# Kernel optimization log

Hardware: AMD Instinct MI355X
Metric: run time of the kernel (lower is better)

## Reference

```python
import jax, jax.numpy as jnp
from jax import lax
import numpy as np

INPUT_DIM = 1024; ENT_DIM = 256; KEY_DIM = 32; FUNC_DIM = 256; HID = 32
NUM_LAYERS = 1; UNIT_TYPE_DIM = 259; MAX_ENT = 64; B = 256; N = 512
NEG = 1e9

def _ln(x, g, b, eps=1e-5):
    m = x.mean(-1, keepdims=True)
    v = ((x - m) ** 2).mean(-1, keepdims=True)
    return (x - m) / jnp.sqrt(v + eps) * g + b

def setup_inputs() -> dict:
    key = jax.random.key(0)
    ks = jax.random.split(key, 16)
    def lin(k, i, o, s=0.02):
        return jax.random.normal(k, (i, o), jnp.float32) * s, jnp.zeros((o,), jnp.float32)
    p = {}
    p['key_fc_w'], p['key_fc_b'] = lin(ks[0], ENT_DIM, KEY_DIM)
    p['func_fc_w'], p['func_fc_b'] = lin(ks[1], UNIT_TYPE_DIM, FUNC_DIM)
    p['fc1_w'], p['fc1_b'] = lin(ks[2], INPUT_DIM, FUNC_DIM)
    p['fc2_w'], p['fc2_b'] = lin(ks[3], FUNC_DIM, KEY_DIM)
    p['embed_fc_w'], p['embed_fc_b'] = lin(ks[4], KEY_DIM, INPUT_DIM)
    p['lstm_wx'] = jax.random.normal(ks[5], (NUM_LAYERS, KEY_DIM, 4 * HID), jnp.float32) * 0.05
    p['lstm_wh'] = jax.random.normal(ks[6], (NUM_LAYERS, HID, 4 * HID), jnp.float32) * 0.05
    p['lstm_b'] = jnp.zeros((NUM_LAYERS, 4 * HID), jnp.float32)
    p['lstm_ln_gx'] = jnp.ones((NUM_LAYERS, 4 * HID), jnp.float32)
    p['lstm_ln_bx'] = jnp.zeros((NUM_LAYERS, 4 * HID), jnp.float32)
    p['lstm_ln_gh'] = jnp.ones((NUM_LAYERS, 4 * HID), jnp.float32)
    p['lstm_ln_bh'] = jnp.zeros((NUM_LAYERS, 4 * HID), jnp.float32)
    inp = {
        'embedding': jax.random.normal(ks[7], (B, INPUT_DIM), jnp.float32),
        'available_unit_type_mask': (jax.random.uniform(ks[8], (B, UNIT_TYPE_DIM)) < 0.5).astype(jnp.float32),
        'available_units_mask': jnp.ones((B, N), jnp.float32),
        'entity_embedding': jax.random.normal(ks[9], (B, N, ENT_DIM), jnp.float32),
        'temperature': jnp.float32(1.0),
    }
    inp.update(p)
    return inp

def reference(embedding, available_unit_type_mask, available_units_mask, entity_embedding,
              temperature, key_fc_w, key_fc_b, func_fc_w, func_fc_b, fc1_w, fc1_b,
              fc2_w, fc2_b, embed_fc_w, embed_fc_b, lstm_wx, lstm_wh, lstm_b,
              lstm_ln_gx, lstm_ln_bx, lstm_ln_gh, lstm_ln_bh):
    relu = jax.nn.relu
    # _get_key: [B,N,KEY] + end-flag row of zeros -> [B,N+1,KEY]
    key = entity_embedding @ key_fc_w + key_fc_b
    key = jnp.concatenate([key, jnp.zeros((B, 1, KEY_DIM), key.dtype)], axis=1)
    end_idx = N
    # _get_init_query
    func_embed = relu(available_unit_type_mask @ func_fc_w + func_fc_b)
    x0 = relu(embedding @ fc1_w + fc1_b)
    x0 = relu((x0 + func_embed) @ fc2_w + fc2_b)  # [B, KEY_DIM]
    mask0 = jnp.concatenate([available_units_mask, jnp.ones((B, 1), available_units_mask.dtype)], axis=1)

    h0 = jnp.zeros((NUM_LAYERS, B, HID), key.dtype)
    c0 = jnp.zeros((NUM_LAYERS, B, HID), key.dtype)
    units0 = jnp.zeros((B, N + 1), jnp.int32)
    done0 = jnp.zeros((B,), bool)
    rng0 = jax.random.key(42)

    def step(carry, _):
        x, h, c, mask, units, done, rng = carry
        xi = x
        hs, cs = [], []
        for l in range(NUM_LAYERS):  # LN-LSTM, gate order i,f,o,u (DI-engine)
            gate = (_ln(xi @ lstm_wx[l], lstm_ln_gx[l], lstm_ln_bx[l])
                    + _ln(h[l] @ lstm_wh[l], lstm_ln_gh[l], lstm_ln_bh[l]) + lstm_b[l])
            i_g, f_g, o_g, u_g = jnp.split(gate, 4, axis=-1)
            cl = jax.nn.sigmoid(f_g) * c[l] + jax.nn.sigmoid(i_g) * jnp.tanh(u_g)
            hl = jax.nn.sigmoid(o_g) * jnp.tanh(cl)
            hs.append(hl); cs.append(cl); xi = hl
        h_new = jnp.stack(hs); c_new = jnp.stack(cs)
        q = (xi[:, None, :] * key).mean(-1)          # [B, N+1] pointer scores
        q = q - (1.0 - mask) * NEG
        rng, sk = jax.random.split(rng)
        idx = jax.random.categorical(sk, q / temperature, axis=-1)  # [B]
        is_end = idx == end_idx
        active = jnp.logical_not(done)
        sel = active & jnp.logical_not(is_end)
        onehot = jax.nn.one_hot(idx, N + 1, dtype=mask.dtype)
        units = jnp.where(sel[:, None] & (onehot > 0.5), 1, units)
        mask = jnp.where(sel[:, None], mask * (1.0 - onehot), mask)
        done = done | (active & is_end)
        return (xi, h_new, c_new, mask, units, done, rng), (q, active)

    carry, (logits, valid) = lax.scan(step, (x0, h0, c0, mask0, units0, done0, rng0), None, length=MAX_ENT)
    units = carry[4]
    emb_sel = (units[..., None].astype(key.dtype) * key).mean(axis=1)  # [B, KEY_DIM]
    emb_sel = emb_sel @ embed_fc_w + embed_fc_b
    return logits, valid, units, embedding + emb_sel
```

## Files before the change

kernel.cpp:

```cpp
#include <hip/hip_runtime.h>
#include <stdint.h>
#include <stddef.h>

#define JAX_PARTITIONABLE 1

#define B_   256
#define N_   512
#define NP_  513
#define KROW 516
#define T_   64
#define CS   4
#define NCH  16
#define NEGC 1e9f

__host__ __device__ __forceinline__ void tf2x32(uint32_t k0, uint32_t k1,
    uint32_t x0, uint32_t x1, uint32_t& o0, uint32_t& o1) {
  const uint32_t k2 = k0 ^ k1 ^ 0x1BD11BDAu;
#define TFR(r) { x0 += x1; x1 = (x1 << (r)) | (x1 >> (32 - (r))); x1 ^= x0; }
  x0 += k0; x1 += k1;
  TFR(13) TFR(15) TFR(26) TFR(6)
  x0 += k1; x1 += k2 + 1u;
  TFR(17) TFR(29) TFR(16) TFR(24)
  x0 += k2; x1 += k0 + 2u;
  TFR(13) TFR(15) TFR(26) TFR(6)
  x0 += k0; x1 += k1 + 3u;
  TFR(17) TFR(29) TFR(16) TFR(24)
  x0 += k1; x1 += k2 + 4u;
  TFR(13) TFR(15) TFR(26) TFR(6)
  x0 += k2; x1 += k0 + 5u;
#undef TFR
  o0 = x0; o1 = x1;
}

struct SkKeys { uint32_t k[128]; };

static SkKeys compute_chain() {
  SkKeys s;
  uint32_t r0 = 0u, r1 = 42u;
  for (int t = 0; t < 64; ++t) {
#if JAX_PARTITIONABLE
    uint32_t a0, a1, b0, b1;
    tf2x32(r0, r1, 0u, 0u, a0, a1);
    tf2x32(r0, r1, 0u, 1u, b0, b1);
    s.k[2*t] = b0; s.k[2*t+1] = b1;
    r0 = a0; r1 = a1;
#else
    uint32_t p0, p1, q0, q1;
    tf2x32(r0, r1, 0u, 2u, p0, p1);
    tf2x32(r0, r1, 1u, 3u, q0, q1);
    s.k[2*t] = p1; s.k[2*t+1] = q1;
    r0 = p0; r1 = q0;
#endif
  }
  return s;
}

__device__ __forceinline__ float gumbel_draw(uint32_t k0, uint32_t k1, int b, int n) {
  uint32_t bits;
#if JAX_PARTITIONABLE
  uint32_t j = (uint32_t)(b * NP_ + n);
  uint32_t o0, o1; tf2x32(k0, k1, 0u, j, o0, o1);
  bits = o0 ^ o1;
#else
  int j = b * NP_ + n;
  uint32_t o0, o1;
  if (j < 65664) { tf2x32(k0, k1, (uint32_t)j, (uint32_t)(j + 65664), o0, o1); bits = o0; }
  else           { tf2x32(k0, k1, (uint32_t)(j - 65664), (uint32_t)j, o0, o1); bits = o1; }
#endif
  float f = __uint_as_float((bits >> 9) | 0x3F800000u) - 1.0f;
  const float TINY = 1.17549435e-38f;
  float u = fmaxf(TINY, f + TINY);
  return -logf(-logf(u));
}

__device__ __forceinline__ float sigm(float x) {
  return 0.5f + 0.5f * tanhf(0.5f * x);
}

__device__ __forceinline__ void bar_lds() {
  asm volatile("s_waitcnt lgkmcnt(0)\n\ts_barrier" ::: "memory");
}

#define OFF_KEY   0
#define OFF_H     16512
#define OFF_Q     18560
#define OFF_G     22688
#define OFF_UNITS 33008
#define OFF_SK    33524
#define OFF_ES    33652
#define OFF_PART  33684
#define OFF_T     34196
#define OFF_X0    34452
#define LDS_FLOATS 34484

__global__ void __launch_bounds__(512, 2)
suh_fused(const float* __restrict__ emb, const float* __restrict__ autm,
          const float* __restrict__ aum, const float* __restrict__ ent,
          const float* __restrict__ temp_p,
          const float* __restrict__ key_w, const float* __restrict__ key_b,
          const float* __restrict__ func_w, const float* __restrict__ func_b,
          const float* __restrict__ fc1_w, const float* __restrict__ fc1_b,
          const float* __restrict__ fc2_w, const float* __restrict__ fc2_b,
          const float* __restrict__ emb_w, const float* __restrict__ emb_b,
          const float* __restrict__ wx, const float* __restrict__ wh,
          const float* __restrict__ lstm_bb,
          const float* __restrict__ ln_gx, const float* __restrict__ ln_bx,
          const float* __restrict__ ln_gh, const float* __restrict__ ln_bh,
          float* __restrict__ out_logits, float* __restrict__ out_valid,
          float* __restrict__ out_units, float* __restrict__ out_final,
          SkKeys sk)
{
  extern __shared__ __align__(16) float sm[];
  int* smi = (int*)sm;
  const int b   = blockIdx.x;
  const int tid = threadIdx.x;
  const int L   = tid - 64;

  const float temp = temp_p[0];

  if (tid < 256) {
    float a = 0.f;
    const float* e = emb + (size_t)b * 1024;
    #pragma unroll 8
    for (int k = 0; k < 1024; ++k) a += e[k] * fc1_w[k * 256 + tid];
    a = fmaxf(a + fc1_b[tid], 0.f);
    float f = 0.f;
    const float* m = autm + (size_t)b * 259;
    for (int k = 0; k < 259; ++k) f += m[k] * func_w[k * 256 + tid];
    f = fmaxf(f + func_b[tid], 0.f);
    sm[OFF_T + tid] = a + f;
  } else {
    if (tid < 384) smi[OFF_SK + (tid - 256)] = (int)sk.k[tid - 256];
    if (tid >= 480) sm[OFF_KEY + (tid - 480) * KROW + N_] = 0.f;
  }
  __syncthreads();

  if (tid < 32) {
    float s = 0.f;
    #pragma unroll 8
    for (int m2 = 0; m2 < 256; ++m2) s += sm[OFF_T + m2] * fc2_w[m2 * 32 + tid];
    sm[OFF_X0 + tid] = fmaxf(s + fc2_b[tid], 0.f);
  }
  __syncthreads();

  float kr0[32], kr1[32];
  float mreg[8], ureg[8];
  float m512 = 1.0f;
  int done_reg = 0;

  auto qprep = [&](int cc, int qs) {
    const int qb = OFF_Q + qs * (CS * 516);
    #pragma unroll 1
    for (int tl = 0; tl < CS; ++tl) {
      const int hb = OFF_H + (cc * CS + tl) * 32;
      float hv[32];
      #pragma unroll
      for (int r = 0; r < 8; ++r) {
        float4 v = *(const float4*)&sm[hb + r * 4];
        hv[r*4] = v.x; hv[r*4+1] = v.y; hv[r*4+2] = v.z; hv[r*4+3] = v.w;
      }
      float a0 = 0.f;
      #pragma unroll
      for (int k = 0; k < 32; ++k) a0 += hv[k] * kr0[k];
      sm[qb + tl * 516 + L] = a0 * (1.0f / 32.0f);
      if (L < 64) {
        float a1 = 0.f;
        #pragma unroll
        for (int k = 0; k < 32; ++k) a1 += hv[k] * kr1[k];
        sm[qb + tl * 516 + L + 448] = a1 * (1.0f / 32.0f);
      }
    }
  };
  auto gprep = [&](int cc, int gs) {
    const int gb = OFF_G + gs * (CS * 516);
    #pragma unroll 1
    for (int i = 0; i < 5; ++i) {
      const int idx = i * 448 + L;
      if (idx < CS * 512) {
        const int tl = idx >> 9, n = idx & 511;
        const int t = cc * CS + tl;
        sm[gb + tl * 516 + n] =
            gumbel_draw((uint32_t)smi[OFF_SK + 2*t], (uint32_t)smi[OFF_SK + 2*t + 1], b, n);
      }
    }
    if (L < CS) {
      const int t = cc * CS + L;
      sm[gb + L * 516 + N_] =
          gumbel_draw((uint32_t)smi[OFF_SK + 2*t], (uint32_t)smi[OFF_SK + 2*t + 1], b, N_);
    }
  };

  if (tid < 64) {
    float wxr0[32], wxr1[32], whr0[32], whr1[32];
    #pragma unroll
    for (int k = 0; k < 32; ++k) {
      wxr0[k] = wx[k * 128 + tid];
      wxr1[k] = wx[k * 128 + 64 + tid];
      whr0[k] = wh[k * 128 + tid];
      whr1[k] = wh[k * 128 + 64 + tid];
    }
    #pragma unroll
    for (int k = 0; k < 32; ++k) {
      asm volatile("" : "+v"(wxr0[k]), "+v"(wxr1[k]), "+v"(whr0[k]), "+v"(whr1[k]));
    }
    const float gxg0 = ln_gx[tid], gxg1 = ln_gx[tid + 64];
    const float gxb0 = ln_bx[tid], gxb1 = ln_bx[tid + 64];
    const float ghg0 = ln_gh[tid], ghg1 = ln_gh[tid + 64];
    const float ghb0 = ln_bh[tid], ghb1 = ln_bh[tid + 64];
    const float lb0  = lstm_bb[tid], lb1 = lstm_bb[tid + 64];

    float xf[32];
    #pragma unroll
    for (int r = 0; r < 8; ++r) {
      float4 v = *(const float4*)&sm[OFF_X0 + r * 4];
      xf[r*4] = v.x; xf[r*4+1] = v.y; xf[r*4+2] = v.z; xf[r*4+3] = v.w;
    }
    float creg = 0.f;

    #pragma unroll 1
    for (int t = 0; t < T_; ++t) {
      float a0 = 0.f, a1 = 0.f, b0 = 0.f, b1 = 0.f;
      #pragma unroll
      for (int k = 0; k < 32; ++k) { a0 += xf[k] * wxr0[k]; a1 += xf[k] * wxr1[k]; }
      if (t > 0) {
        #pragma unroll
        for (int k = 0; k < 32; ++k) { b0 += xf[k] * whr0[k]; b1 += xf[k] * whr1[k]; }
      }
      float sx = a0 + a1, sh = b0 + b1;
      for (int off = 32; off; off >>= 1) {
        sx += __shfl_down(sx, off);
        sh += __shfl_down(sh, off);
      }
      float mx  = __shfl(sx, 0) * (1.0f / 128.0f);
      float mh2 = __shfl(sh, 0) * (1.0f / 128.0f);
      float dx0 = a0 - mx, dx1 = a1 - mx;
      float dh0 = b0 - mh2, dh1 = b1 - mh2;
      float ssx = dx0 * dx0 + dx1 * dx1;
      float ssh = dh0 * dh0 + dh1 * dh1;
      for (int off = 32; off; off >>= 1) {
        ssx += __shfl_down(ssx, off);
        ssh += __shfl_down(ssh, off);
      }
      float vx = __shfl(ssx, 0) * (1.0f / 128.0f);
      float vh = __shfl(ssh, 0) * (1.0f / 128.0f);
      float rx = 1.0f / sqrtf(vx + 1e-5f);
      float rh = 1.0f / sqrtf(vh + 1e-5f);
      float lnx0 = dx0 * rx * gxg0 + gxb0;
      float lnx1 = dx1 * rx * gxg1 + gxb1;
      float lnh0 = dh0 * rh * ghg0 + ghb0;
      float lnh1 = dh1 * rh * ghg1 + ghb1;
      float g0 = lnx0 + lnh0 + lb0;
      float g1 = lnx1 + lnh1 + lb1;
      float fq = __shfl(g0, tid + 32);
      float uq = __shfl(g1, tid + 32);
      float cN = sigm(fq) * creg + sigm(g0) * tanhf(uq);
      float hN = sigm(g1) * tanhf(cN);
      creg = cN;
      if (tid < 32) sm[OFF_H + t * 32 + tid] = hN;
      #pragma unroll
      for (int k = 0; k < 32; ++k) xf[k] = __shfl(hN, k);
    }
  } else {
    const float4* kw4 = (const float4*)key_w;
    {
      const float4* er = (const float4*)(ent + ((size_t)b * N_ + L) * 256);
      float acc[32];
      #pragma unroll
      for (int c = 0; c < 32; ++c) acc[c] = 0.f;
      #pragma unroll 1
      for (int k4 = 0; k4 < 64; ++k4) {
        float4 ev = er[k4];
        float e4[4] = {ev.x, ev.y, ev.z, ev.w};
        #pragma unroll
        for (int j = 0; j < 4; ++j) {
          const int k = k4 * 4 + j;
          #pragma unroll
          for (int c4 = 0; c4 < 8; ++c4) {
            float4 w = kw4[k * 8 + c4];
            acc[c4*4+0] += e4[j] * w.x;
            acc[c4*4+1] += e4[j] * w.y;
            acc[c4*4+2] += e4[j] * w.z;
            acc[c4*4+3] += e4[j] * w.w;
          }
        }
      }
      #pragma unroll
      for (int c = 0; c < 32; ++c) {
        kr0[c] = acc[c] + key_b[c];
        sm[OFF_KEY + c * KROW + L] = kr0[c];
      }
    }
    if (L < 64) {
      const int n = L + 448;
      const float4* er = (const float4*)(ent + ((size_t)b * N_ + n) * 256);
      float acc[32];
      #pragma unroll
      for (int c = 0; c < 32; ++c) acc[c] = 0.f;
      #pragma unroll 1
      for (int k4 = 0; k4 < 64; ++k4) {
        float4 ev = er[k4];
        float e4[4] = {ev.x, ev.y, ev.z, ev.w};
        #pragma unroll
        for (int j = 0; j < 4; ++j) {
          const int k = k4 * 4 + j;
          #pragma unroll
          for (int c4 = 0; c4 < 8; ++c4) {
            float4 w = kw4[k * 8 + c4];
            acc[c4*4+0] += e4[j] * w.x;
            acc[c4*4+1] += e4[j] * w.y;
            acc[c4*4+2] += e4[j] * w.z;
            acc[c4*4+3] += e4[j] * w.w;
          }
        }
      }
      #pragma unroll
      for (int c = 0; c < 32; ++c) {
        kr1[c] = acc[c] + key_b[c];
        sm[OFF_KEY + c * KROW + n] = kr1[c];
      }
    }
    #pragma unroll
    for (int k = 0; k < 32; ++k) {
      asm volatile("" : "+v"(kr0[k]), "+v"(kr1[k]));
    }
    #pragma unroll 1
    for (int cc = 0; cc < 4; ++cc) gprep(cc, cc);
  }
  __syncthreads();

  if (tid < 64) {
    #pragma unroll
    for (int j = 0; j < 8; ++j) {
      mreg[j] = aum[(size_t)b * N_ + tid + 64 * j];
      ureg[j] = 0.f;
    }
  } else {
    qprep(0, 0);
  }
  bar_lds();

  for (int c = 0; c < NCH; ++c) {
    if (tid < 64) {
      const int qbase = OFF_Q + (c & 1) * (CS * 516);
      const int gbase = OFF_G + (c % 5) * (CS * 516);
      #pragma unroll 1
      for (int tl = 0; tl < CS; ++tl) {
        const int t = c * CS + tl;
        float* lrow = out_logits + ((size_t)t * B_ + b) * NP_;
        float bv = 0.f; int bi = 0;
        #pragma unroll
        for (int j = 0; j < 8; ++j) {
          const int n = tid + 64 * j;
          float q = sm[qbase + tl * 516 + n] - (1.0f - mreg[j]) * NEGC;
          lrow[n] = q;
          float v = q / temp + sm[gbase + tl * 516 + n];
          if (j == 0) { bv = v; bi = n; }
          else if (v > bv) { bv = v; bi = n; }
        }
        if (tid == 0) {
          float q = -(1.0f - m512) * NEGC;
          lrow[N_] = q;
          float v = q / temp + sm[gbase + tl * 516 + N_];
          if (v > bv) { bv = v; bi = N_; }
        }
        for (int off = 32; off; off >>= 1) {
          float ov = __shfl_down(bv, off);
          int   oi = __shfl_down(bi, off);
          if (ov > bv || (ov == bv && oi < bi)) { bv = ov; bi = oi; }
        }
        const int sel_i = __shfl(bi, 0);
        const int active = !done_reg;
        const int is_end = (sel_i == N_);
        if (tid == 0) out_valid[(size_t)t * B_ + b] = active ? 1.0f : 0.0f;
        if (active && !is_end) {
          #pragma unroll
          for (int j = 0; j < 8; ++j)
            if (tid + 64 * j == sel_i) { mreg[j] = 0.0f; ureg[j] = 1.0f; }
        }
        if (active && is_end) done_reg = 1;
      }
    } else {
      if (c + 1 < NCH) qprep(c + 1, (c + 1) & 1);
      if (c + 4 < NCH) gprep(c + 4, (c + 4) % 5);
    }
    bar_lds();
  }

  if (tid < 64) {
    #pragma unroll
    for (int j = 0; j < 8; ++j) sm[OFF_UNITS + tid + 64 * j] = ureg[j];
    if (tid == 0) sm[OFF_UNITS + N_] = 0.f;
  }
  __syncthreads();

  {
    const int g = tid >> 5, cc = tid & 31;
    float p = 0.f;
    const int n0 = g * 32;
    for (int nn = 0; nn < 32; ++nn) {
      const int n = n0 + nn;
      p += sm[OFF_UNITS + n] * sm[OFF_KEY + cc * KROW + n];
    }
    if (g == 15) p += sm[OFF_UNITS + N_] * sm[OFF_KEY + cc * KROW + N_];
    sm[OFF_PART + g * 32 + cc] = p;
  }
  for (int n = tid; n < NP_; n += 512) out_units[(size_t)b * NP_ + n] = sm[OFF_UNITS + n];
  __syncthreads();
  if (tid < 32) {
    float s = 0.f;
    #pragma unroll
    for (int g = 0; g < 16; ++g) s += sm[OFF_PART + g * 32 + tid];
    sm[OFF_ES + tid] = s / 513.0f;
  }
  __syncthreads();
  {
    const float* e = emb + (size_t)b * 1024;
    for (int d = tid; d < 1024; d += 512) {
      float a = 0.f;
      #pragma unroll
      for (int k = 0; k < 32; ++k) a += sm[OFF_ES + k] * emb_w[k * 1024 + d];
      out_final[(size_t)b * 1024 + d] = e[d] + a + emb_b[d];
    }
  }
}

extern "C" void kernel_launch(void* const* d_in, const int* in_sizes, int n_in,
                              void* d_out, int out_size, void* d_ws, size_t ws_size,
                              hipStream_t stream) {
  (void)in_sizes; (void)n_in; (void)d_ws; (void)ws_size; (void)out_size;
  const float* emb    = (const float*)d_in[0];
  const float* autm   = (const float*)d_in[1];
  const float* aum    = (const float*)d_in[2];
  const float* ent    = (const float*)d_in[3];
  const float* temp   = (const float*)d_in[4];
  const float* key_w  = (const float*)d_in[5];
  const float* key_b  = (const float*)d_in[6];
  const float* func_w = (const float*)d_in[7];
  const float* func_b = (const float*)d_in[8];
  const float* fc1_w  = (const float*)d_in[9];
  const float* fc1_b  = (const float*)d_in[10];
  const float* fc2_w  = (const float*)d_in[11];
  const float* fc2_b  = (const float*)d_in[12];
  const float* emb_w  = (const float*)d_in[13];
  const float* emb_b  = (const float*)d_in[14];
  const float* wx     = (const float*)d_in[15];
  const float* wh     = (const float*)d_in[16];
  const float* lb     = (const float*)d_in[17];
  const float* gxg    = (const float*)d_in[18];
  const float* gxb    = (const float*)d_in[19];
  const float* ghg    = (const float*)d_in[20];
  const float* ghb    = (const float*)d_in[21];
  float* out = (float*)d_out;

  const size_t OFF_V = (size_t)T_ * B_ * NP_;
  const size_t OFF_U = OFF_V + (size_t)T_ * B_;
  const size_t OFF_F = OFF_U + (size_t)B_ * NP_;

  SkKeys sk = compute_chain();

  suh_fused<<<dim3(B_), dim3(512), LDS_FLOATS * sizeof(float), stream>>>(
      emb, autm, aum, ent, temp, key_w, key_b, func_w, func_b,
      fc1_w, fc1_b, fc2_w, fc2_b, emb_w, emb_b,
      wx, wh, lb, gxg, gxb, ghg, ghb,
      out, out + OFF_V, out + OFF_U, out + OFF_F, sk);
}
```

Measured before the change: 242.4 us.

## Split fused kernel into precompute, LSTM and sampling kernels via workspace

The single fused kernel becomes three launches. The first computes the key projection and the initial MLP input into global workspace using all 512 threads. The second runs the 64-step LSTM recurrence in a 64-thread block per batch row and writes h to workspace. The third reloads keys and h into LDS and runs the Gumbel sampling loop. This removes the intra-block overlap of LSTM with key projection, aiming for a better thread balance in the key projection. In exchange it adds launch overhead, global round trips for about 17 MB of keys, and a serialized LSTM kernel that runs with very low occupancy.

Result: slower. 299.5 us (+23.6%).

```diff
diff --git a/kernel.cpp b/kernel.cpp
--- a/kernel.cpp
+++ b/kernel.cpp
@@ -81,42 +81,22 @@
   asm volatile("s_waitcnt lgkmcnt(0)\n\ts_barrier" ::: "memory");
 }
 
-#define OFF_KEY   0
-#define OFF_H     16512
-#define OFF_Q     18560
-#define OFF_G     22688
-#define OFF_UNITS 33008
-#define OFF_SK    33524
-#define OFF_ES    33652
-#define OFF_PART  33684
-#define OFF_T     34196
-#define OFF_X0    34452
-#define LDS_FLOATS 34484
+#define WS_KEY 0
+#define WS_X0  (B_ * 32 * KROW)
+#define WS_H   (WS_X0 + B_ * 32)
 
 __global__ void __launch_bounds__(512, 2)
-suh_fused(const float* __restrict__ emb, const float* __restrict__ autm,
-          const float* __restrict__ aum, const float* __restrict__ ent,
-          const float* __restrict__ temp_p,
-          const float* __restrict__ key_w, const float* __restrict__ key_b,
-          const float* __restrict__ func_w, const float* __restrict__ func_b,
-          const float* __restrict__ fc1_w, const float* __restrict__ fc1_b,
-          const float* __restrict__ fc2_w, const float* __restrict__ fc2_b,
-          const float* __restrict__ emb_w, const float* __restrict__ emb_b,
-          const float* __restrict__ wx, const float* __restrict__ wh,
-          const float* __restrict__ lstm_bb,
-          const float* __restrict__ ln_gx, const float* __restrict__ ln_bx,
-          const float* __restrict__ ln_gh, const float* __restrict__ ln_bh,
-          float* __restrict__ out_logits, float* __restrict__ out_valid,
-          float* __restrict__ out_units, float* __restrict__ out_final,
-          SkKeys sk)
+k_pre(const float* __restrict__ emb, const float* __restrict__ autm,
+      const float* __restrict__ ent,
+      const float* __restrict__ key_w, const float* __restrict__ key_b,
+      const float* __restrict__ func_w, const float* __restrict__ func_b,
+      const float* __restrict__ fc1_w, const float* __restrict__ fc1_b,
+      const float* __restrict__ fc2_w, const float* __restrict__ fc2_b,
+      float* __restrict__ ws)
 {
-  extern __shared__ __align__(16) float sm[];
-  int* smi = (int*)sm;
+  __shared__ float smT[256];
   const int b   = blockIdx.x;
   const int tid = threadIdx.x;
-  const int L   = tid - 64;
-
-  const float temp = temp_p[0];
 
   if (tid < 256) {
     float a = 0.f;
@@ -128,146 +108,18 @@
     const float* m = autm + (size_t)b * 259;
     for (int k = 0; k < 259; ++k) f += m[k] * func_w[k * 256 + tid];
     f = fmaxf(f + func_b[tid], 0.f);
-    sm[OFF_T + tid] = a + f;
+    smT[tid] = a + f;
   } else {
-    if (tid < 384) smi[OFF_SK + (tid - 256)] = (int)sk.k[tid - 256];
-    if (tid >= 480) sm[OFF_KEY + (tid - 480) * KROW + N_] = 0.f;
-  }
-  __syncthreads();
-
-  if (tid < 32) {
-    float s = 0.f;
-    #pragma unroll 8
-    for (int m2 = 0; m2 < 256; ++m2) s += sm[OFF_T + m2] * fc2_w[m2 * 32 + tid];
-    sm[OFF_X0 + tid] = fmaxf(s + fc2_b[tid], 0.f);
-  }
-  __syncthreads();
-
-  float kr0[32], kr1[32];
-  float mreg[8], ureg[8];
-  float m512 = 1.0f;
-  int done_reg = 0;
-
-  auto qprep = [&](int cc, int qs) {
-    const int qb = OFF_Q + qs * (CS * 516);
+    const int i = tid - 256;
+    const float4* kw4 = (const float4*)key_w;
     #pragma unroll 1
-    for (int tl = 0; tl < CS; ++tl) {
-      const int hb = OFF_H + (cc * CS + tl) * 32;
-      float hv[32];
-      #pragma unroll
-      for (int r = 0; r < 8; ++r) {
-        float4 v = *(const float4*)&sm[hb + r * 4];
-        hv[r*4] = v.x; hv[r*4+1] = v.y; hv[r*4+2] = v.z; hv[r*4+3] = v.w;
-      }
-      float a0 = 0.f;
-      #pragma unroll
-      for (int k = 0; k < 32; ++k) a0 += hv[k] * kr0[k];
-      sm[qb + tl * 516 + L] = a0 * (1.0f / 32.0f);
-      if (L < 64) {
-        float a1 = 0.f;
-        #pragma unroll
-        for (int k = 0; k < 32; ++k) a1 += hv[k] * kr1[k];
-        sm[qb + tl * 516 + L + 448] = a1 * (1.0f / 32.0f);
-      }
-    }
-  };
-  auto gprep = [&](int cc, int gs) {
-    const int gb = OFF_G + gs * (CS * 516);
-    #pragma unroll 1
-    for (int i = 0; i < 5; ++i) {
-      const int idx = i * 448 + L;
-      if (idx < CS * 512) {
-        const int tl = idx >> 9, n = idx & 511;
-        const int t = cc * CS + tl;
-        sm[gb + tl * 516 + n] =
-            gumbel_draw((uint32_t)smi[OFF_SK + 2*t], (uint32_t)smi[OFF_SK + 2*t + 1], b, n);
-      }
-    }
-    if (L < CS) {
-      const int t = cc * CS + L;
-      sm[gb + L * 516 + N_] =
-          gumbel_draw((uint32_t)smi[OFF_SK + 2*t], (uint32_t)smi[OFF_SK + 2*t + 1], b, N_);
-    }
-  };
-
-  if (tid < 64) {
-    float wxr0[32], wxr1[32], whr0[32], whr1[32];
-    #pragma unroll
-    for (int k = 0; k < 32; ++k) {
-      wxr0[k] = wx[k * 128 + tid];
-      wxr1[k] = wx[k * 128 + 64 + tid];
-      whr0[k] = wh[k * 128 + tid];
-      whr1[k] = wh[k * 128 + 64 + tid];
-    }
-    #pragma unroll
-    for (int k = 0; k < 32; ++k) {
-      asm volatile("" : "+v"(wxr0[k]), "+v"(wxr1[k]), "+v"(whr0[k]), "+v"(whr1[k]));
-    }
-    const float gxg0 = ln_gx[tid], gxg1 = ln_gx[tid + 64];
-    const float gxb0 = ln_bx[tid], gxb1 = ln_bx[tid + 64];
-    const float ghg0 = ln_gh[tid], ghg1 = ln_gh[tid + 64];
-    const float ghb0 = ln_bh[tid], ghb1 = ln_bh[tid + 64];
-    const float lb0  = lstm_bb[tid], lb1 = lstm_bb[tid + 64];
-
-    float xf[32];
-    #pragma unroll
-    for (int r = 0; r < 8; ++r) {
-      float4 v = *(const float4*)&sm[OFF_X0 + r * 4];
-      xf[r*4] = v.x; xf[r*4+1] = v.y; xf[r*4+2] = v.z; xf[r*4+3] = v.w;
-    }
-    float creg = 0.f;
-
-    #pragma unroll 1
-    for (int t = 0; t < T_; ++t) {
-      float a0 = 0.f, a1 = 0.f, b0 = 0.f, b1 = 0.f;
-      #pragma unroll
-      for (int k = 0; k < 32; ++k) { a0 += xf[k] * wxr0[k]; a1 += xf[k] * wxr1[k]; }
-      if (t > 0) {
-        #pragma unroll
-        for (int k = 0; k < 32; ++k) { b0 += xf[k] * whr0[k]; b1 += xf[k] * whr1[k]; }
-      }
-      float sx = a0 + a1, sh = b0 + b1;
-      for (int off = 32; off; off >>= 1) {
-        sx += __shfl_down(sx, off);
-        sh += __shfl_down(sh, off);
-      }
-      float mx  = __shfl(sx, 0) * (1.0f / 128.0f);
-      float mh2 = __shfl(sh, 0) * (1.0f / 128.0f);
-      float dx0 = a0 - mx, dx1 = a1 - mx;
-      float dh0 = b0 - mh2, dh1 = b1 - mh2;
-      float ssx = dx0 * dx0 + dx1 * dx1;
-      float ssh = dh0 * dh0 + dh1 * dh1;
-      for (int off = 32; off; off >>= 1) {
-        ssx += __shfl_down(ssx, off);
-        ssh += __shfl_down(ssh, off);
-      }
-      float vx = __shfl(ssx, 0) * (1.0f / 128.0f);
-      float vh = __shfl(ssh, 0) * (1.0f / 128.0f);
-      float rx = 1.0f / sqrtf(vx + 1e-5f);
-      float rh = 1.0f / sqrtf(vh + 1e-5f);
-      float lnx0 = dx0 * rx * gxg0 + gxb0;
-      float lnx1 = dx1 * rx * gxg1 + gxb1;
-      float lnh0 = dh0 * rh * ghg0 + ghb0;
-      float lnh1 = dh1 * rh * ghg1 + ghb1;
-      float g0 = lnx0 + lnh0 + lb0;
-      float g1 = lnx1 + lnh1 + lb1;
-      float fq = __shfl(g0, tid + 32);
-      float uq = __shfl(g1, tid + 32);
-      float cN = sigm(fq) * creg + sigm(g0) * tanhf(uq);
-      float hN = sigm(g1) * tanhf(cN);
-      creg = cN;
-      if (tid < 32) sm[OFF_H + t * 32 + tid] = hN;
-      #pragma unroll
-      for (int k = 0; k < 32; ++k) xf[k] = __shfl(hN, k);
-    }
-  } else {
-    const float4* kw4 = (const float4*)key_w;
-    {
-      const float4* er = (const float4*)(ent + ((size_t)b * N_ + L) * 256);
+    for (int rnd = 0; rnd < 2; ++rnd) {
+      const int n = i + rnd * 256;
+      const float4* er = (const float4*)(ent + ((size_t)b * N_ + n) * 256);
       float acc[32];
       #pragma unroll
       for (int c = 0; c < 32; ++c) acc[c] = 0.f;
-      #pragma unroll 1
+      #pragma unroll 4
       for (int k4 = 0; k4 < 64; ++k4) {
         float4 ev = er[k4];
         float e4[4] = {ev.x, ev.y, ev.z, ev.w};
@@ -285,48 +137,188 @@
         }
       }
       #pragma unroll
-      for (int c = 0; c < 32; ++c) {
-        kr0[c] = acc[c] + key_b[c];
-        sm[OFF_KEY + c * KROW + L] = kr0[c];
+      for (int c = 0; c < 32; ++c)
+        ws[WS_KEY + ((size_t)(b * 32 + c)) * KROW + n] = acc[c] + key_b[c];
+    }
+    if (i < 32) ws[WS_KEY + ((size_t)(b * 32 + i)) * KROW + N_] = 0.f;
+  }
+  __syncthreads();
+
+  if (tid < 32) {
+    float s = 0.f;
+    #pragma unroll 8
+    for (int m2 = 0; m2 < 256; ++m2) s += smT[m2] * fc2_w[m2 * 32 + tid];
+    ws[WS_X0 + b * 32 + tid] = fmaxf(s + fc2_b[tid], 0.f);
+  }
+}
+
+__global__ void __launch_bounds__(64, 1)
+k_beta(const float* __restrict__ wx, const float* __restrict__ wh,
+       const float* __restrict__ lstm_bb,
+       const float* __restrict__ ln_gx, const float* __restrict__ ln_bx,
+       const float* __restrict__ ln_gh, const float* __restrict__ ln_bh,
+       float* __restrict__ ws)
+{
+  const int b   = blockIdx.x;
+  const int tid = threadIdx.x;
+
+  float wxr0[32], wxr1[32], whr0[32], whr1[32];
+  #pragma unroll
+  for (int k = 0; k < 32; ++k) {
+    wxr0[k] = wx[k * 128 + tid];
+    wxr1[k] = wx[k * 128 + 64 + tid];
+    whr0[k] = wh[k * 128 + tid];
+    whr1[k] = wh[k * 128 + 64 + tid];
+  }
+  #pragma unroll
+  for (int k = 0; k < 32; ++k) {
+    asm volatile("" : "+v"(wxr0[k]), "+v"(wxr1[k]), "+v"(whr0[k]), "+v"(whr1[k]));
+  }
+  const float gxg0 = ln_gx[tid], gxg1 = ln_gx[tid + 64];
+  const float gxb0 = ln_bx[tid], gxb1 = ln_bx[tid + 64];
+  const float ghg0 = ln_gh[tid], ghg1 = ln_gh[tid + 64];
+  const float ghb0 = ln_bh[tid], ghb1 = ln_bh[tid + 64];
+  const float lb0  = lstm_bb[tid], lb1 = lstm_bb[tid + 64];
+
+  float xf[32];
+  {
+    const float* x0g = ws + WS_X0 + b * 32;
+    #pragma unroll
+    for (int r = 0; r < 8; ++r) {
+      float4 v = *(const float4*)(x0g + r * 4);
+      xf[r*4] = v.x; xf[r*4+1] = v.y; xf[r*4+2] = v.z; xf[r*4+3] = v.w;
+    }
+  }
+  float creg = 0.f;
+  float* Hout = ws + WS_H + (size_t)b * (T_ * 32);
+
+  #pragma unroll 1
+  for (int t = 0; t < T_; ++t) {
+    float a0 = 0.f, a1 = 0.f, b0 = 0.f, b1 = 0.f;
+    #pragma unroll
+    for (int k = 0; k < 32; ++k) { a0 += xf[k] * wxr0[k]; a1 += xf[k] * wxr1[k]; }
+    if (t > 0) {
+      #pragma unroll
+      for (int k = 0; k < 32; ++k) { b0 += xf[k] * whr0[k]; b1 += xf[k] * whr1[k]; }
+    }
+    float sx = a0 + a1, sh = b0 + b1;
+    for (int off = 32; off; off >>= 1) {
+      sx += __shfl_down(sx, off);
+      sh += __shfl_down(sh, off);
+    }
+    float mx  = __shfl(sx, 0) * (1.0f / 128.0f);
+    float mh2 = __shfl(sh, 0) * (1.0f / 128.0f);
+    float dx0 = a0 - mx, dx1 = a1 - mx;
+    float dh0 = b0 - mh2, dh1 = b1 - mh2;
+    float ssx = dx0 * dx0 + dx1 * dx1;
+    float ssh = dh0 * dh0 + dh1 * dh1;
+    for (int off = 32; off; off >>= 1) {
+      ssx += __shfl_down(ssx, off);
+      ssh += __shfl_down(ssh, off);
+    }
+    float vx = __shfl(ssx, 0) * (1.0f / 128.0f);
+    float vh = __shfl(ssh, 0) * (1.0f / 128.0f);
+    float rx = 1.0f / sqrtf(vx + 1e-5f);
+    float rh = 1.0f / sqrtf(vh + 1e-5f);
+    float lnx0 = dx0 * rx * gxg0 + gxb0;
+    float lnx1 = dx1 * rx * gxg1 + gxb1;
+    float lnh0 = dh0 * rh * ghg0 + ghb0;
+    float lnh1 = dh1 * rh * ghg1 + ghb1;
+    float g0 = lnx0 + lnh0 + lb0;
+    float g1 = lnx1 + lnh1 + lb1;
+    float fq = __shfl(g0, tid + 32);
+    float uq = __shfl(g1, tid + 32);
+    float cN = sigm(fq) * creg + sigm(g0) * tanhf(uq);
+    float hN = sigm(g1) * tanhf(cN);
+    creg = cN;
+    if (tid < 32) Hout[t * 32 + tid] = hN;
+    #pragma unroll
+    for (int k = 0; k < 32; ++k) xf[k] = __shfl(hN, k);
+  }
+}
+
+#define OFF_KEY   0
+#define OFF_H     16512
+#define OFF_Q     18560
+#define OFF_G     22688
+#define OFF_UNITS 33008
+#define OFF_SK    33524
+#define OFF_ES    33652
+#define OFF_PART  33684
+#define LDS_FLOATS 34196
+
+__global__ void __launch_bounds__(512, 2)
+k_sample(const float* __restrict__ ws_ro,
+         const float* __restrict__ aum, const float* __restrict__ temp_p,
+         const float* __restrict__ emb,
+         const float* __restrict__ emb_w, const float* __restrict__ emb_b,
+         float* __restrict__ out_logits, float* __restrict__ out_valid,
+         float* __restrict__ out_units, float* __restrict__ out_final,
+         SkKeys sk)
+{
+  extern __shared__ __align__(16) float sm[];
+  int* smi = (int*)sm;
+  const int b   = blockIdx.x;
+  const int tid = threadIdx.x;
+  const int L   = tid - 64;
+
+  const float temp = temp_p[0];
+
+  {
+    const float4* kv = (const float4*)(ws_ro + WS_KEY + (size_t)b * (32 * KROW));
+    for (int i = tid; i < (32 * KROW) / 4; i += 512) ((float4*)sm)[i] = kv[i];
+    const float4* hv = (const float4*)(ws_ro + WS_H + (size_t)b * (T_ * 32));
+    if (tid < 512) ((float4*)(sm + OFF_H))[tid] = hv[tid];
+    if (tid < 128) smi[OFF_SK + tid] = (int)sk.k[tid];
+  }
+  __syncthreads();
+
+  float kr0[32], kr1[32];
+  float mreg[8], ureg[8];
+  float m512 = 1.0f;
+  int done_reg = 0;
+
+  auto qprep = [&](int cc, int qs) {
+    const int qb = OFF_Q + qs * (CS * 516);
+    #pragma unroll 1
+    for (int tl = 0; tl < CS; ++tl) {
+      const int hb = OFF_H + (cc * CS + tl) * 32;
+      float hv[32];
+      #pragma unroll
+      for (int r = 0; r < 8; ++r) {
+        float4 v = *(const float4*)&sm[hb + r * 4];
+        hv[r*4] = v.x; hv[r*4+1] = v.y; hv[r*4+2] = v.z; hv[r*4+3] = v.w;
       }
-    }
-    if (L < 64) {
-      const int n = L + 448;
-      const float4* er = (const float4*)(ent + ((size_t)b * N_ + n) * 256);
-      float acc[32];
-      #pragma unroll
-      for (int c = 0; c < 32; ++c) acc[c] = 0.f;
-      #pragma unroll 1
-      for (int k4 = 0; k4 < 64; ++k4) {
-        float4 ev = er[k4];
-        float e4[4] = {ev.x, ev.y, ev.z, ev.w};
+      float a0 = 0.f;
+      #pragma unroll
+      for (int k = 0; k < 32; ++k) a0 += hv[k] * kr0[k];
+      sm[qb + tl * 516 + L] = a0 * (1.0f / 32.0f);
+      if (L < 64) {
+        float a1 = 0.f;
         #pragma unroll
-        for (int j = 0; j < 4; ++j) {
-          const int k = k4 * 4 + j;
-          #pragma unroll
-          for (int c4 = 0; c4 < 8; ++c4) {
-            float4 w = kw4[k * 8 + c4];
-            acc[c4*4+0] += e4[j] * w.x;
-            acc[c4*4+1] += e4[j] * w.y;
-            acc[c4*4+2] += e4[j] * w.z;
-            acc[c4*4+3] += e4[j] * w.w;
-          }
-        }
+        for (int k = 0; k < 32; ++k) a1 += hv[k] * kr1[k];
+        sm[qb + tl * 516 + L + 448] = a1 * (1.0f / 32.0f);
       }
-      #pragma unroll
-      for (int c = 0; c < 32; ++c) {
-        kr1[c] = acc[c] + key_b[c];
-        sm[OFF_KEY + c * KROW + n] = kr1[c];
+    }
+  };
+  auto gprep = [&](int cc, int gs) {
+    const int gb = OFF_G + gs * (CS * 516);
+    #pragma unroll 1
+    for (int i = 0; i < 5; ++i) {
+      const int idx = i * 448 + L;
+      if (idx < CS * 512) {
+        const int tl = idx >> 9, n = idx & 511;
+        const int t = cc * CS + tl;
+        sm[gb + tl * 516 + n] =
+            gumbel_draw((uint32_t)smi[OFF_SK + 2*t], (uint32_t)smi[OFF_SK + 2*t + 1], b, n);
       }
     }
-    #pragma unroll
-    for (int k = 0; k < 32; ++k) {
-      asm volatile("" : "+v"(kr0[k]), "+v"(kr1[k]));
-    }
-    #pragma unroll 1
-    for (int cc = 0; cc < 4; ++cc) gprep(cc, cc);
-  }
-  __syncthreads();
+    if (L < CS) {
+      const int t = cc * CS + L;
+      sm[gb + L * 516 + N_] =
+          gumbel_draw((uint32_t)smi[OFF_SK + 2*t], (uint32_t)smi[OFF_SK + 2*t + 1], b, N_);
+    }
+  };
 
   if (tid < 64) {
     #pragma unroll
@@ -335,6 +327,14 @@
       ureg[j] = 0.f;
     }
   } else {
+    #pragma unroll
+    for (int c = 0; c < 32; ++c) kr0[c] = sm[OFF_KEY + c * KROW + L];
+    if (L < 64) {
+      #pragma unroll
+      for (int c = 0; c < 32; ++c) kr1[c] = sm[OFF_KEY + c * KROW + L + 448];
+    }
+    #pragma unroll 1
+    for (int cc = 0; cc < 4; ++cc) gprep(cc, cc);
     qprep(0, 0);
   }
   bar_lds();
@@ -427,7 +427,7 @@
 extern "C" void kernel_launch(void* const* d_in, const int* in_sizes, int n_in,
                               void* d_out, int out_size, void* d_ws, size_t ws_size,
                               hipStream_t stream) {
-  (void)in_sizes; (void)n_in; (void)d_ws; (void)ws_size; (void)out_size;
+  (void)in_sizes; (void)n_in; (void)ws_size; (void)out_size;
   const float* emb    = (const float*)d_in[0];
   const float* autm   = (const float*)d_in[1];
   const float* aum    = (const float*)d_in[2];
@@ -451,6 +451,7 @@
   const float* ghg    = (const float*)d_in[20];
   const float* ghb    = (const float*)d_in[21];
   float* out = (float*)d_out;
+  float* ws  = (float*)d_ws;
 
   const size_t OFF_V = (size_t)T_ * B_ * NP_;
   const size_t OFF_U = OFF_V + (size_t)T_ * B_;
@@ -458,9 +459,14 @@
 
   SkKeys sk = compute_chain();
 
-  suh_fused<<<dim3(B_), dim3(512), LDS_FLOATS * sizeof(float), stream>>>(
-      emb, autm, aum, ent, temp, key_w, key_b, func_w, func_b,
-      fc1_w, fc1_b, fc2_w, fc2_b, emb_w, emb_b,
-      wx, wh, lb, gxg, gxb, ghg, ghb,
+  k_pre<<<dim3(B_), dim3(512), 0, stream>>>(
+      emb, autm, ent, key_w, key_b, func_w, func_b,
+      fc1_w, fc1_b, fc2_w, fc2_b, ws);
+
+  k_beta<<<dim3(B_), dim3(64), 0, stream>>>(
+      wx, wh, lb, gxg, gxb, ghg, ghb, ws);
+
+  k_sample<<<dim3(B_), dim3(512), LDS_FLOATS * sizeof(float), stream>>>(
+      ws, aum, temp, emb, emb_w, emb_b,
       out, out + OFF_V, out + OFF_U, out + OFF_F, sk);
 }
```
